# Performance work log

Hardware: AMD Instinct MI355X
Metric: run time of the kernel (lower is better)

The kernel has to match this reference:

```python
import jax, jax.numpy as jnp
import numpy as np

ALPHA = 2.0  # spikingjelly surrogate.Erf default alpha

@jax.custom_vjp
def erf_spike(x):
    # spiking forward: heaviside(x); backward uses Erf surrogate gradient
    return (x >= 0).astype(x.dtype)

def _erf_spike_fwd(x):
    return erf_spike(x), x

def _erf_spike_bwd(x, g):
    return (g * jnp.exp(-(x * ALPHA) ** 2) * (ALPHA / np.sqrt(np.pi)),)

erf_spike.defvjp(_erf_spike_fwd, _erf_spike_bwd)

L, T, B, C, H, N_LAYERS = 256, 4, 32, 256, 256, 2

def setup_inputs() -> dict:
    key = jax.random.key(0)
    ks = jax.random.split(key, 8)
    k = 1.0 / np.sqrt(H)  # uniform(-sqrt(1/H), sqrt(1/H)) init
    u = lambda kk, shape: jax.random.uniform(kk, shape, jnp.float32, -k, k)
    return {
        "x": jax.random.normal(ks[0], (L, T, B, C), jnp.float32),
        "W_ih0": u(ks[1], (4 * H, C)),
        "W_hh0": u(ks[2], (4 * H, H)),
        "b0": u(ks[3], (4 * H,)),
        "W_ih1": u(ks[4], (4 * H, H)),
        "W_hh1": u(ks[5], (4 * H, H)),
        "b1": u(ks[6], (4 * H,)),
    }

def _run_layer(inp, W_ih, W_hh, b):
    # inp: [L, T, B, Cin] -> fold T,B into one batch axis for the scan
    Ls, Ts, Bs = inp.shape[0], inp.shape[1], inp.shape[2]
    Hs = W_hh.shape[1]
    xin = inp.reshape(Ls, Ts * Bs, -1)

    def step(carry, x_t):
        h, c = carry
        gates = x_t @ W_ih.T + h @ W_hh.T + b  # [TB, 4H]
        i, f, g, o = jnp.split(gates, 4, axis=-1)
        i = erf_spike(i)
        f = erf_spike(f)
        g = erf_spike(g)
        o = erf_spike(o)
        c = f * c + i * g
        # torch.clamp_max_ under no_grad: value clamp, straight-through grad
        c = c + jax.lax.stop_gradient(jnp.minimum(c, 1.0) - c)
        h = o * c
        return (h, c), h

    h0 = jnp.zeros((Ts * Bs, Hs), inp.dtype)
    (h, c), out = jax.lax.scan(step, (h0, h0), xin)
    return (out.reshape(Ls, Ts, Bs, Hs),
            h.reshape(Ts, Bs, Hs),
            c.reshape(Ts, Bs, Hs))

def reference(x, W_ih0, W_hh0, b0, W_ih1, W_hh1, b1):
    out0, h0, c0 = _run_layer(x, W_ih0, W_hh0, b0)
    out1, h1, c1 = _run_layer(out0, W_ih1, W_hh1, b1)
    state_h = jnp.stack([h0, h1])  # [N, T, B, H]
    state_c = jnp.stack([c0, c1])
    return out1, (state_h, state_c)
```

## Files before the change

kernel.cpp:

```cpp
#include <hip/hip_runtime.h>
#include <math.h>

typedef _Float16 half8 __attribute__((ext_vector_type(8)));
typedef _Float16 half4v __attribute__((ext_vector_type(4)));
typedef float floatx4 __attribute__((ext_vector_type(4)));
typedef unsigned long long u64;

#define MFMA16(a, b, c) __builtin_amdgcn_mfma_f32_16x16x32_f16((a), (b), (c), 0, 0, 0)
#define AARG __ATOMIC_RELAXED, __HIP_MEMORY_SCOPE_AGENT

static constexpr float C11 = 4.8828125e-4f;
static constexpr int SLOTS = 257;
static constexpr int LSTRIDE = SLOTS * 8 * 128;

__device__ u64 g_exch[2 * LSTRIDE];
__device__ _Float16 g_xhi[8388608];
__device__ _Float16 g_xlo[8388608];
__device__ float g_phi[33554432];
__device__ _Float16 g_plo[33554432];

__global__ __launch_bounds__(256) void zero_k() {
  unsigned i = blockIdx.x * 256 + threadIdx.x;
  if (i < 2 * LSTRIDE) g_exch[i] = 0;
}

__device__ __forceinline__ u64 ald(const u64* p) { return __hip_atomic_load(p, AARG); }
__device__ __forceinline__ void ast(u64* p, u64 v) { __hip_atomic_store(p, v, AARG); }

__device__ __forceinline__ void split16(float v, _Float16& hi, _Float16& lo) {
  _Float16 h = (fabsf(v) < 6.103515625e-05f) ? (_Float16)0.0f : (_Float16)v;
  hi = h;
  lo = (_Float16)((v - (float)h) * 2048.0f);
}

__global__ __launch_bounds__(256) void presplit_k(const float* __restrict__ x) {
  int i = (blockIdx.x * 256 + threadIdx.x) * 8;
  floatx4 a = *(const floatx4*)(x + i);
  floatx4 b = *(const floatx4*)(x + i + 4);
  half8 hi, lo;
#pragma unroll
  for (int e = 0; e < 4; ++e) { _Float16 p, q; split16(a[e], p, q); hi[e] = p; lo[e] = q; }
#pragma unroll
  for (int e = 0; e < 4; ++e) { _Float16 p, q; split16(b[e], p, q); hi[4 + e] = p; lo[4 + e] = q; }
  *(half8*)(g_xhi + i) = hi;
  *(half8*)(g_xlo + i) = lo;
}

__global__ __launch_bounds__(256) void gemm0_k(const float* __restrict__ wih) {
  const int tid = threadIdx.x, lane = tid & 63, wv = tid >> 6;
  const int m16 = lane & 15, l16 = lane >> 4;
  const int bi = blockIdx.x;
  const int lc = bi >> 6, g = (bi >> 3) & 7, kwg = bi & 7;

  half8 WH[2][8], WL[2][8];
#pragma unroll
  for (int t2 = 0; t2 < 2; ++t2) {
    int grow = wv * 256 + 32 * kwg + t2 * 16 + m16;
#pragma unroll
    for (int q = 0; q < 8; ++q) {
      const float* src = wih + (size_t)grow * 256 + 32 * q + 8 * l16;
      floatx4 v0 = *(const floatx4*)src;
      floatx4 v1 = *(const floatx4*)(src + 4);
      half8 hi, lo;
#pragma unroll
      for (int e = 0; e < 4; ++e) { _Float16 p, q2; split16(v0[e], p, q2); hi[e] = p; lo[e] = q2; }
#pragma unroll
      for (int e = 0; e < 4; ++e) { _Float16 p, q2; split16(v1[e], p, q2); hi[4 + e] = p; lo[4 + e] = q2; }
      WH[t2][q] = hi;
      WL[t2][q] = lo;
    }
  }
#pragma unroll 1
  for (int l = lc * 32; l < lc * 32 + 32; ++l) {
    size_t base = ((size_t)l * 128 + 16 * g + m16) * 256 + 8 * l16;
    half8 xh[8], xl[8];
#pragma unroll
    for (int q = 0; q < 8; ++q) {
      xh[q] = *(const half8*)(g_xhi + base + 32 * q);
      xl[q] = *(const half8*)(g_xlo + base + 32 * q);
    }
    floatx4 zz = {0.f, 0.f, 0.f, 0.f};
    floatx4 A0[2], A1[2], A2[2];
    A0[0] = A0[1] = zz; A1[0] = A1[1] = zz; A2[0] = A2[1] = zz;
#pragma unroll
    for (int q = 0; q < 8; ++q)
#pragma unroll
      for (int t2 = 0; t2 < 2; ++t2) {
        A0[t2] = MFMA16(xh[q], WH[t2][q], A0[t2]);
        A1[t2] = MFMA16(xh[q], WL[t2][q], A1[t2]);
        A1[t2] = MFMA16(xl[q], WH[t2][q], A1[t2]);
        A2[t2] = MFMA16(xl[q], WL[t2][q], A2[t2]);
      }
#pragma unroll
    for (int t2 = 0; t2 < 2; ++t2) {
      size_t off = ((((((size_t)l * 8 + g) * 8 + kwg) * 4 + wv) * 2 + t2) * 64 + lane) * 4;
      *(floatx4*)(g_phi + off) = A0[t2];
      half4v hv;
#pragma unroll
      for (int r = 0; r < 4; ++r) hv[r] = (_Float16)(A1[t2][r] + C11 * A2[t2][r]);
      *(half4v*)(g_plo + off) = hv;
    }
  }
}

template <int LAYER>
__device__ void scan_body(_Float16* lut, float* ihb, unsigned* hw, u64* spike,
                          const float* __restrict__ wih,
                          const float* __restrict__ whh,
                          const float* __restrict__ bias,
                          float* __restrict__ dout, int g, int kwg) {
  const int tid = threadIdx.x;
  const int lane = tid & 63;
  const int wv = tid >> 6;
  const bool prod = wv < 4;
  const int gate = wv & 3;
  const int m16 = lane & 15;
  const int l16 = lane >> 4;

  u64* exch0 = g_exch;
  u64* exchMy = g_exch + LAYER * LSTRIDE;

  if (tid < 256) {
#pragma unroll
    for (int e = 0; e < 8; ++e)
      lut[tid * 8 + e] = ((tid >> e) & 1) ? (_Float16)1.0f : (_Float16)0.0f;
  }

  half8 FH[2][8], FL[2][8];
  if (!prod || LAYER == 1) {
    const float* wsrc = prod ? wih : whh;
#pragma unroll
    for (int t2 = 0; t2 < 2; ++t2) {
      int grow = gate * 256 + 32 * kwg + t2 * 16 + m16;
#pragma unroll
      for (int q = 0; q < 8; ++q) {
        const float* src = wsrc + (size_t)grow * 256 + 32 * q + 8 * l16;
        floatx4 v0 = *(const floatx4*)src;
        floatx4 v1 = *(const floatx4*)(src + 4);
        half8 hi, lo;
#pragma unroll
        for (int e = 0; e < 4; ++e) { _Float16 p, q2; split16(v0[e], p, q2); hi[e] = p; lo[e] = q2; }
#pragma unroll
        for (int e = 0; e < 4; ++e) { _Float16 p, q2; split16(v1[e], p, q2); hi[4 + e] = p; lo[4 + e] = q2; }
        FH[t2][q] = hi;
        FL[t2][q] = lo;
      }
    }
  }
  float bl[2];
#pragma unroll
  for (int t2 = 0; t2 < 2; ++t2) bl[t2] = bias[gate * 256 + 32 * kwg + t2 * 16 + m16];

  floatx4 ihA0[2], ihA1[2];
  floatx4 phv[2];
  half4v plv[2];
  u64 xwA[8];
  unsigned xw[8];
  u64 cst = 0;
  int polls = 0;
  const int POLL_MAX = 1 << 22;

  auto issue_pl = [&](int l) {
#pragma unroll
    for (int t2 = 0; t2 < 2; ++t2) {
      size_t off = ((((((size_t)l * 8 + g) * 8 + kwg) * 4 + gate) * 2 + t2) * 64 + lane) * 4;
      phv[t2] = *(const floatx4*)(g_phi + off);
      plv[t2] = *(const half4v*)(g_plo + off);
    }
  };
  auto issue_xw = [&](int tag) {
    const u64* page = exch0 + (size_t)tag * 1024 + g * 128 + m16;
#pragma unroll
    for (int q = 0; q < 8; ++q) xwA[q] = ald(page + q * 16);
  };
  auto consume_xw = [&](int tag) {
    bool ok = true;
#pragma unroll
    for (int q = 0; q < 8; ++q) ok = ok && ((unsigned)xwA[q] == (unsigned)tag);
    if (!__all(ok)) {
      const u64* page = exch0 + (size_t)tag * 1024 + g * 128 + m16;
      for (;;) {
#pragma unroll
        for (int q = 0; q < 8; ++q) xwA[q] = ald(page + q * 16);
        bool k2 = true;
#pragma unroll
        for (int q = 0; q < 8; ++q) k2 = k2 && ((unsigned)xwA[q] == (unsigned)tag);
        if (__all(k2)) break;
        if (++polls > POLL_MAX) break;
      }
    }
#pragma unroll
    for (int q = 0; q < 8; ++q) xw[q] = (unsigned)(xwA[q] >> 32);
  };
  auto ih_mfma = [&]() {
    floatx4 zz = {0.f, 0.f, 0.f, 0.f};
    ihA0[0] = ihA0[1] = zz;
    ihA1[0] = ihA1[1] = zz;
#pragma unroll
    for (int q = 0; q < 8; ++q) {
      unsigned byt = (xw[q] >> (8 * l16)) & 0xFFu;
      half8 ah = *(const half8*)(lut + byt * 8);
#pragma unroll
      for (int t2 = 0; t2 < 2; ++t2) {
        ihA0[t2] = MFMA16(ah, FH[t2][q], ihA0[t2]);
        ihA1[t2] = MFMA16(ah, FL[t2][q], ihA1[t2]);
      }
    }
  };
  auto gather16 = [&](u64 v) -> unsigned {
    unsigned a0 = __shfl((unsigned)v, lane & 3);
    unsigned a1 = __shfl((unsigned)(v >> 32), lane & 3);
    unsigned b0 = __shfl((unsigned)v, 4 + (lane & 3));
    unsigned b1 = __shfl((unsigned)(v >> 32), 4 + (lane & 3));
    u64 A = ((u64)a1 << 32) | a0;
    u64 B = ((u64)b1 << 32) | b0;
    int sh = 16 * ((lane & 15) >> 2);
    return (unsigned)((A >> sh) & 0xFFFFull) |
           ((unsigned)((B >> sh) & 0xFFFFull) << 16);
  };

  if (prod) {
    if constexpr (LAYER == 0) {
      issue_pl(0);
    } else {
      issue_xw(1);
      consume_xw(1);
      ih_mfma();
      issue_xw(2);
    }
  }
  __syncthreads();

#pragma unroll 1
  for (int l = 0; l < 256; ++l) {
    if (prod) {
      float* bp = ihb + ((gate * 2 + 0) * 8) * 64 + lane;
#pragma unroll
      for (int t2 = 0; t2 < 2; ++t2) {
        float* b2 = ihb + ((gate * 2 + t2) * 8) * 64 + lane;
        if constexpr (LAYER == 0) {
#pragma unroll
          for (int r = 0; r < 4; ++r) {
            b2[r * 64] = phv[t2][r];
            b2[(4 + r) * 64] = (float)plv[t2][r];
          }
        } else {
#pragma unroll
          for (int r = 0; r < 4; ++r) {
            b2[r * 64] = ihA0[t2][r];
            b2[(4 + r) * 64] = ihA1[t2][r];
          }
        }
      }
      (void)bp;
    } else if (wv == 4 && l > 0) {
      const u64* pa = exchMy + (size_t)l * 1024 + g * 128 + 2 * lane;
      u64 v0 = ald(pa), v1 = ald(pa + 1);
      for (;;) {
        if (__all(((unsigned)v0 == (unsigned)l) && ((unsigned)v1 == (unsigned)l))) break;
        v0 = ald(pa);
        v1 = ald(pa + 1);
        if (++polls > POLL_MAX) break;
      }
      hw[2 * lane] = (unsigned)(v0 >> 32);
      hw[2 * lane + 1] = (unsigned)(v1 >> 32);
    }
    __syncthreads();
    if (prod) {
      if (l < 255) {
        if constexpr (LAYER == 0) {
          issue_pl(l + 1);
        } else {
          consume_xw(l + 2);
          ih_mfma();
          if (l + 3 <= 256) issue_xw(l + 3);
        }
      }
    } else {
      floatx4 C0[2], C1[2];
#pragma unroll
      for (int t2 = 0; t2 < 2; ++t2) {
        const float* b2 = ihb + ((gate * 2 + t2) * 8) * 64 + lane;
#pragma unroll
        for (int r = 0; r < 4; ++r) {
          C0[t2][r] = b2[r * 64];
          C1[t2][r] = b2[(4 + r) * 64];
        }
      }
      if (l > 0) {
#pragma unroll
        for (int q = 0; q < 8; ++q) {
          unsigned mw = hw[q * 16 + m16];
          unsigned byt = (mw >> (8 * l16)) & 0xFFu;
          half8 af = *(const half8*)(lut + byt * 8);
          C0[0] = MFMA16(af, FH[0][q], C0[0]);
          C0[1] = MFMA16(af, FH[1][q], C0[1]);
          C1[0] = MFMA16(af, FL[0][q], C1[0]);
          C1[1] = MFMA16(af, FL[1][q], C1[1]);
        }
      }
      u64 bal[2][4];
#pragma unroll
      for (int r = 0; r < 4; ++r) {
        float p0 = C0[0][r] + bl[0] + C11 * C1[0][r];
        float p1 = C0[1][r] + bl[1] + C11 * C1[1][r];
        bal[0][r] = __ballot(p0 >= 0.0f);
        bal[1][r] = __ballot(p1 >= 0.0f);
      }
      if (lane == 0) {
#pragma unroll
        for (int t2 = 0; t2 < 2; ++t2)
#pragma unroll
          for (int r = 0; r < 4; ++r) spike[gate * 8 + t2 * 4 + r] = bal[t2][r];
      }
    }
    __syncthreads();
    {
      int idx = lane & 7;
      u64 iS = spike[idx], fS = spike[8 + idx];
      u64 gS = spike[16 + idx], oS = spike[24 + idx];
      cst = (fS & cst) | (iS & gS);
      (void)oS;
    }
    u64 hS = spike[24 + (lane & 7)] & cst;
    if (wv == 0) {
      unsigned hu = gather16(hS);
      if (lane < 16)
        ast(exchMy + (size_t)(l + 1) * 1024 + g * 128 + kwg * 16 + lane,
            ((u64)hu << 32) | (unsigned)(l + 1));
    }
    if (LAYER == 1 && wv == 1) {
      unsigned hu = gather16(hS);
      if (lane < 16) {
        float* frow = dout + ((size_t)l * 128 + 16 * g + lane) * 256 + 32 * kwg;
#pragma unroll
        for (int c4 = 0; c4 < 8; ++c4) {
          floatx4 v;
#pragma unroll
          for (int j = 0; j < 4; ++j) v[j] = ((hu >> (c4 * 4 + j)) & 1) ? 1.0f : 0.0f;
          *(floatx4*)(frow + c4 * 4) = v;
        }
      }
    }
    if (l == 255 && wv == 2) {
      unsigned hu = gather16(hS);
      unsigned cu = gather16(cst);
      if (lane < 16) {
        float* shp = dout + 8388608 + LAYER * 32768 +
                     (size_t)(16 * g + lane) * 256 + 32 * kwg;
        float* scp = shp + 65536;
#pragma unroll
        for (int c4 = 0; c4 < 8; ++c4) {
          floatx4 vh, vc;
#pragma unroll
          for (int j = 0; j < 4; ++j) {
            vh[j] = ((hu >> (c4 * 4 + j)) & 1) ? 1.0f : 0.0f;
            vc[j] = ((cu >> (c4 * 4 + j)) & 1) ? 1.0f : 0.0f;
          }
          *(floatx4*)(shp + c4 * 4) = vh;
          *(floatx4*)(scp + c4 * 4) = vc;
        }
      }
    }
  }
}

__global__ __launch_bounds__(512, 2) void spike_scan(
    const float* __restrict__ wih1, const float* __restrict__ whh0,
    const float* __restrict__ whh1, const float* __restrict__ b0,
    const float* __restrict__ b1, float* __restrict__ dout) {
  __shared__ __align__(16) _Float16 lut[256 * 8];
  __shared__ __align__(16) float ihb[4 * 2 * 8 * 64];
  __shared__ unsigned hw[128];
  __shared__ u64 spike[32];

  int bi = blockIdx.x;
  int g = bi & 7;
  int kwg = (bi >> 3) & 7;
  if ((bi >> 6) == 0)
    scan_body<0>(lut, ihb, hw, spike, (const float*)nullptr, whh0, b0, dout, g, kwg);
  else
    scan_body<1>(lut, ihb, hw, spike, wih1, whh1, b1, dout, g, kwg);
}

extern "C" void kernel_launch(void* const* d_in, const int* in_sizes, int n_in,
                              void* d_out, int out_size, void* d_ws, size_t ws_size,
                              hipStream_t stream) {
  (void)in_sizes; (void)n_in; (void)out_size; (void)d_ws; (void)ws_size;
  const float* x = (const float*)d_in[0];
  const float* wih0 = (const float*)d_in[1];
  const float* whh0 = (const float*)d_in[2];
  const float* b0 = (const float*)d_in[3];
  const float* wih1 = (const float*)d_in[4];
  const float* whh1 = (const float*)d_in[5];
  const float* b1 = (const float*)d_in[6];
  float* dout = (float*)d_out;

  zero_k<<<2056, 256, 0, stream>>>();
  presplit_k<<<4096, 256, 0, stream>>>(x);
  gemm0_k<<<512, 256, 0, stream>>>(wih0);
  spike_scan<<<128, 512, 0, stream>>>(wih1, whh0, whh1, b0, b1, dout);
}
```

Baseline: 651.7 us.

## Interleave two batch groups per workgroup to hide cross-block exchange latency

```diff
diff --git a/kernel.cpp b/kernel.cpp
--- a/kernel.cpp
+++ b/kernel.cpp
@@ -108,7 +108,7 @@
                           const float* __restrict__ wih,
                           const float* __restrict__ whh,
                           const float* __restrict__ bias,
-                          float* __restrict__ dout, int g, int kwg) {
+                          float* __restrict__ dout, int gA, int gB, int kwg) {
   const int tid = threadIdx.x;
   const int lane = tid & 63;
   const int wv = tid >> 6;
@@ -151,16 +151,16 @@
 #pragma unroll
   for (int t2 = 0; t2 < 2; ++t2) bl[t2] = bias[gate * 256 + 32 * kwg + t2 * 16 + m16];
 
-  floatx4 ihA0[2], ihA1[2];
-  floatx4 phv[2];
-  half4v plv[2];
-  u64 xwA[8];
+  floatx4 phvA[2], phvB[2];
+  half4v plvA[2], plvB[2];
+  u64 xwAtA[8], xwAtB[8];
+  floatx4 ihR0A[2], ihR1A[2], ihR0B[2], ihR1B[2];
   unsigned xw[8];
-  u64 cst = 0;
+  u64 cstA = 0, cstB = 0;
   int polls = 0;
   const int POLL_MAX = 1 << 22;
 
-  auto issue_pl = [&](int l) {
+  auto issue_pl = [&](int l, int g, floatx4(&phv)[2], half4v(&plv)[2]) {
 #pragma unroll
     for (int t2 = 0; t2 < 2; ++t2) {
       size_t off = ((((((size_t)l * 8 + g) * 8 + kwg) * 4 + gate) * 2 + t2) * 64 + lane) * 4;
@@ -168,42 +168,42 @@
       plv[t2] = *(const half4v*)(g_plo + off);
     }
   };
-  auto issue_xw = [&](int tag) {
+  auto issue_xw = [&](int tag, int g, u64(&at)[8]) {
     const u64* page = exch0 + (size_t)tag * 1024 + g * 128 + m16;
 #pragma unroll
-    for (int q = 0; q < 8; ++q) xwA[q] = ald(page + q * 16);
-  };
-  auto consume_xw = [&](int tag) {
+    for (int q = 0; q < 8; ++q) at[q] = ald(page + q * 16);
+  };
+  auto consume_xw = [&](int tag, int g, u64(&at)[8]) {
     bool ok = true;
 #pragma unroll
-    for (int q = 0; q < 8; ++q) ok = ok && ((unsigned)xwA[q] == (unsigned)tag);
+    for (int q = 0; q < 8; ++q) ok = ok && ((unsigned)at[q] == (unsigned)tag);
     if (!__all(ok)) {
       const u64* page = exch0 + (size_t)tag * 1024 + g * 128 + m16;
       for (;;) {
 #pragma unroll
-        for (int q = 0; q < 8; ++q) xwA[q] = ald(page + q * 16);
+        for (int q = 0; q < 8; ++q) at[q] = ald(page + q * 16);
         bool k2 = true;
 #pragma unroll
-        for (int q = 0; q < 8; ++q) k2 = k2 && ((unsigned)xwA[q] == (unsigned)tag);
+        for (int q = 0; q < 8; ++q) k2 = k2 && ((unsigned)at[q] == (unsigned)tag);
         if (__all(k2)) break;
         if (++polls > POLL_MAX) break;
       }
     }
 #pragma unroll
-    for (int q = 0; q < 8; ++q) xw[q] = (unsigned)(xwA[q] >> 32);
-  };
-  auto ih_mfma = [&]() {
+    for (int q = 0; q < 8; ++q) xw[q] = (unsigned)(at[q] >> 32);
+  };
+  auto ih_mfma = [&](floatx4(&R0)[2], floatx4(&R1)[2]) {
     floatx4 zz = {0.f, 0.f, 0.f, 0.f};
-    ihA0[0] = ihA0[1] = zz;
-    ihA1[0] = ihA1[1] = zz;
+    R0[0] = R0[1] = zz;
+    R1[0] = R1[1] = zz;
 #pragma unroll
     for (int q = 0; q < 8; ++q) {
       unsigned byt = (xw[q] >> (8 * l16)) & 0xFFu;
       half8 ah = *(const half8*)(lut + byt * 8);
 #pragma unroll
       for (int t2 = 0; t2 < 2; ++t2) {
-        ihA0[t2] = MFMA16(ah, FH[t2][q], ihA0[t2]);
-        ihA1[t2] = MFMA16(ah, FL[t2][q], ihA1[t2]);
+        R0[t2] = MFMA16(ah, FH[t2][q], R0[t2]);
+        R1[t2] = MFMA16(ah, FL[t2][q], R1[t2]);
       }
     }
   };
@@ -219,25 +219,15 @@
            ((unsigned)((B >> sh) & 0xFFFFull) << 16);
   };
 
-  if (prod) {
-    if constexpr (LAYER == 0) {
-      issue_pl(0);
-    } else {
-      issue_xw(1);
-      consume_xw(1);
-      ih_mfma();
-      issue_xw(2);
-    }
-  }
-  __syncthreads();
-
-#pragma unroll 1
-  for (int l = 0; l < 256; ++l) {
+  auto phase = [&](int l, int buf, int g, floatx4(&phv)[2], half4v(&plv)[2],
+                   u64(&xwAt)[8], floatx4(&R0)[2], floatx4(&R1)[2], u64& cst) {
+    unsigned* hwP = hw + buf * 128;
+    u64* spikeP = spike + buf * 32;
+    float* ihbP = ihb + buf * 4096;
     if (prod) {
-      float* bp = ihb + ((gate * 2 + 0) * 8) * 64 + lane;
 #pragma unroll
       for (int t2 = 0; t2 < 2; ++t2) {
-        float* b2 = ihb + ((gate * 2 + t2) * 8) * 64 + lane;
+        float* b2 = ihbP + ((gate * 2 + t2) * 8) * 64 + lane;
         if constexpr (LAYER == 0) {
 #pragma unroll
           for (int r = 0; r < 4; ++r) {
@@ -247,12 +237,11 @@
         } else {
 #pragma unroll
           for (int r = 0; r < 4; ++r) {
-            b2[r * 64] = ihA0[t2][r];
-            b2[(4 + r) * 64] = ihA1[t2][r];
+            b2[r * 64] = R0[t2][r];
+            b2[(4 + r) * 64] = R1[t2][r];
           }
         }
       }
-      (void)bp;
     } else if (wv == 4 && l > 0) {
       const u64* pa = exchMy + (size_t)l * 1024 + g * 128 + 2 * lane;
       u64 v0 = ald(pa), v1 = ald(pa + 1);
@@ -262,25 +251,25 @@
         v1 = ald(pa + 1);
         if (++polls > POLL_MAX) break;
       }
-      hw[2 * lane] = (unsigned)(v0 >> 32);
-      hw[2 * lane + 1] = (unsigned)(v1 >> 32);
+      hwP[2 * lane] = (unsigned)(v0 >> 32);
+      hwP[2 * lane + 1] = (unsigned)(v1 >> 32);
     }
     __syncthreads();
     if (prod) {
       if (l < 255) {
         if constexpr (LAYER == 0) {
-          issue_pl(l + 1);
+          issue_pl(l + 1, g, phv, plv);
         } else {
-          consume_xw(l + 2);
-          ih_mfma();
-          if (l + 3 <= 256) issue_xw(l + 3);
+          consume_xw(l + 2, g, xwAt);
+          ih_mfma(R0, R1);
+          if (l + 3 <= 256) issue_xw(l + 3, g, xwAt);
         }
       }
     } else {
       floatx4 C0[2], C1[2];
 #pragma unroll
       for (int t2 = 0; t2 < 2; ++t2) {
-        const float* b2 = ihb + ((gate * 2 + t2) * 8) * 64 + lane;
+        const float* b2 = ihbP + ((gate * 2 + t2) * 8) * 64 + lane;
 #pragma unroll
         for (int r = 0; r < 4; ++r) {
           C0[t2][r] = b2[r * 64];
@@ -290,7 +279,7 @@
       if (l > 0) {
 #pragma unroll
         for (int q = 0; q < 8; ++q) {
-          unsigned mw = hw[q * 16 + m16];
+          unsigned mw = hwP[q * 16 + m16];
           unsigned byt = (mw >> (8 * l16)) & 0xFFu;
           half8 af = *(const half8*)(lut + byt * 8);
           C0[0] = MFMA16(af, FH[0][q], C0[0]);
@@ -311,18 +300,17 @@
 #pragma unroll
         for (int t2 = 0; t2 < 2; ++t2)
 #pragma unroll
-          for (int r = 0; r < 4; ++r) spike[gate * 8 + t2 * 4 + r] = bal[t2][r];
+          for (int r = 0; r < 4; ++r) spikeP[gate * 8 + t2 * 4 + r] = bal[t2][r];
       }
     }
     __syncthreads();
     {
       int idx = lane & 7;
-      u64 iS = spike[idx], fS = spike[8 + idx];
-      u64 gS = spike[16 + idx], oS = spike[24 + idx];
+      u64 iS = spikeP[idx], fS = spikeP[8 + idx];
+      u64 gS = spikeP[16 + idx];
       cst = (fS & cst) | (iS & gS);
-      (void)oS;
-    }
-    u64 hS = spike[24 + (lane & 7)] & cst;
+    }
+    u64 hS = spikeP[24 + (lane & 7)] & cst;
     if (wv == 0) {
       unsigned hu = gather16(hS);
       if (lane < 16)
@@ -362,25 +350,50 @@
         }
       }
     }
-  }
-}
-
-__global__ __launch_bounds__(512, 2) void spike_scan(
+  };
+
+  if (prod) {
+    if constexpr (LAYER == 0) {
+      issue_pl(0, gA, phvA, plvA);
+      issue_pl(0, gB, phvB, plvB);
+    } else {
+      issue_xw(1, gA, xwAtA);
+      issue_xw(1, gB, xwAtB);
+      consume_xw(1, gA, xwAtA);
+      ih_mfma(ihR0A, ihR1A);
+      issue_xw(2, gA, xwAtA);
+      consume_xw(1, gB, xwAtB);
+      ih_mfma(ihR0B, ihR1B);
+      issue_xw(2, gB, xwAtB);
+    }
+  }
+  __syncthreads();
+
+#pragma unroll 1
+  for (int l = 0; l < 256; ++l) {
+    phase(l, 0, gA, phvA, plvA, xwAtA, ihR0A, ihR1A, cstA);
+    phase(l, 1, gB, phvB, plvB, xwAtB, ihR0B, ihR1B, cstB);
+  }
+}
+
+__global__ __launch_bounds__(512, 1) void spike_scan(
     const float* __restrict__ wih1, const float* __restrict__ whh0,
     const float* __restrict__ whh1, const float* __restrict__ b0,
     const float* __restrict__ b1, float* __restrict__ dout) {
   __shared__ __align__(16) _Float16 lut[256 * 8];
-  __shared__ __align__(16) float ihb[4 * 2 * 8 * 64];
-  __shared__ unsigned hw[128];
-  __shared__ u64 spike[32];
+  __shared__ __align__(16) float ihb[2 * 4 * 2 * 8 * 64];
+  __shared__ unsigned hw[2 * 128];
+  __shared__ u64 spike[2 * 32];
 
   int bi = blockIdx.x;
-  int g = bi & 7;
-  int kwg = (bi >> 3) & 7;
-  if ((bi >> 6) == 0)
-    scan_body<0>(lut, ihb, hw, spike, (const float*)nullptr, whh0, b0, dout, g, kwg);
+  int r = bi & 31;
+  int kwg = r & 7;
+  int pair = r >> 3;
+  int gA = 2 * pair, gB = 2 * pair + 1;
+  if ((bi >> 5) == 0)
+    scan_body<0>(lut, ihb, hw, spike, (const float*)nullptr, whh0, b0, dout, gA, gB, kwg);
   else
-    scan_body<1>(lut, ihb, hw, spike, wih1, whh1, b1, dout, g, kwg);
+    scan_body<1>(lut, ihb, hw, spike, wih1, whh1, b1, dout, gA, gB, kwg);
 }
 
 extern "C" void kernel_launch(void* const* d_in, const int* in_sizes, int n_in,
@@ -399,5 +412,5 @@
   zero_k<<<2056, 256, 0, stream>>>();
   presplit_k<<<4096, 256, 0, stream>>>(x);
   gemm0_k<<<512, 256, 0, stream>>>(wih0);
-  spike_scan<<<128, 512, 0, stream>>>(wih1, whh0, whh1, b0, b1, dout);
-}
+  spike_scan<<<64, 512, 0, stream>>>(wih1, whh0, whh1, b0, b1, dout);
+}
```

After: 1.905 ms. +192.4%, slower.
